# Performance work log

Measured on AMD Instinct MI355X. Metric: run time of the kernel, lower is better.

## Reference

```python
import jax, jax.numpy as jnp
import numpy as np

HQ, HKV, D, RD = 32, 8, 128, 64   # q heads, kv heads, head_dim, rotary_dim
EPS = 1e-6


def _rms_norm(x, w, eps):
    # per-head RMSNorm over last dim (non-gemma: scale by w)
    var = jnp.mean(x * x, axis=-1, keepdims=True)
    return x * jax.lax.rsqrt(var + eps) * w


def _partial_rope(x, c, s, rd):
    # x: [T, H, D]; c/s: [T, rd//2]; NeoX half-split rotation on first rd dims
    x1 = x[..., : rd // 2]
    x2 = x[..., rd // 2 : rd]
    c = c[:, None, :]
    s = s[:, None, :]
    return jnp.concatenate([x1 * c - x2 * s, x2 * c + x1 * s, x[..., rd:]], axis=-1)


def setup_inputs() -> dict:
    key = jax.random.key(0)
    ks = jax.random.split(key, 6)
    B, QL, HID, CACHE = 4, 512, 4096, 512
    T = B * QL
    MAXPOS = 4096
    NPAGES, PS, MP = 256, 16, 64  # total pages, page_size, max pages per seq

    hidden_states = jax.random.normal(ks[0], (T, HID), jnp.float32)
    inv = 1.0 / (10000.0 ** (np.arange(0, RD, 2, dtype=np.float64) / RD))
    ang = np.arange(MAXPOS)[:, None] * inv[None, :]
    cos = jnp.asarray(np.cos(ang), jnp.float32)   # [MAXPOS, RD//2]
    sin = jnp.asarray(np.sin(ang), jnp.float32)
    positions = jnp.tile(CACHE + jnp.arange(QL, dtype=jnp.int32), B)  # [T]
    k_cache = jax.random.normal(ks[1], (NPAGES, PS, HKV, D), jnp.float32)
    v_cache = jax.random.normal(ks[2], (NPAGES, PS, HKV, D), jnp.float32)
    page_table = jnp.arange(B * MP, dtype=jnp.int32).reshape(B, MP)
    cache_seqlens = jnp.full((B,), CACHE, jnp.int32)
    cu_seqlens_q = jnp.arange(B + 1, dtype=jnp.int32) * QL
    qkv_weight = jax.random.normal(ks[3], ((HQ + 2 * HKV) * D, HID), jnp.float32) * 0.02
    o_proj_weight = jax.random.normal(ks[4], (HID, HQ * D), jnp.float32) * 0.02
    q_norm_weight = jnp.ones((D,), jnp.float32)
    k_norm_weight = jnp.ones((D,), jnp.float32)
    return dict(hidden_states=hidden_states, cos=cos, sin=sin, positions=positions,
                k_cache=k_cache, v_cache=v_cache, page_table=page_table,
                cache_seqlens=cache_seqlens, cu_seqlens_q=cu_seqlens_q,
                qkv_weight=qkv_weight, o_proj_weight=o_proj_weight,
                q_norm_weight=q_norm_weight, k_norm_weight=k_norm_weight)


def reference(hidden_states, cos, sin, positions, k_cache, v_cache, page_table,
              cache_seqlens, cu_seqlens_q, qkv_weight, o_proj_weight,
              q_norm_weight, k_norm_weight):
    T = hidden_states.shape[0]
    B = cache_seqlens.shape[0]
    QL = T // B                       # equal-length sequences (extend mode)
    PS = k_cache.shape[1]

    # QKV projection + split
    qkv = hidden_states @ qkv_weight.T
    q, k, v = jnp.split(qkv, [HQ * D, (HQ + HKV) * D], axis=-1)

    # per-head QK RMSNorm (q_norm_weight.shape[0] == head_dim branch)
    q = _rms_norm(q.reshape(T, HQ, D), q_norm_weight, EPS)
    k = _rms_norm(k.reshape(T, HKV, D), k_norm_weight, EPS)
    v = v.reshape(T, HKV, D)

    # partial RoPE
    pc, psn = cos[positions], sin[positions]
    q = _partial_rope(q, pc, psn, RD)
    k = _partial_rope(k, pc, psn, RD)

    # paged KV-cache write: absolute slot = cache_seqlens[b] + j
    pos_abs = cache_seqlens[:, None] + jnp.arange(QL, dtype=jnp.int32)[None, :]  # [B,QL]
    pages = jnp.take_along_axis(page_table, pos_abs // PS, axis=1)
    slots = pos_abs % PS
    k_cache = k_cache.at[pages, slots].set(k.reshape(B, QL, HKV, D))
    v_cache = v_cache.at[pages, slots].set(v.reshape(B, QL, HKV, D))

    # gather per-sequence KV from pages: [B, KV, HKV, D]
    KV = page_table.shape[1] * PS
    keys = k_cache[page_table].reshape(B, KV, HKV, D)
    vals = v_cache[page_table].reshape(B, KV, HKV, D)

    # GQA paged attention with causal mask on absolute positions
    G = HQ // HKV
    qh = q.reshape(B, QL, HKV, G, D)
    scale = 1.0 / np.sqrt(D).astype(np.float32)
    scores = jnp.einsum('bqhgd,bkhd->bhgqk', qh, keys) * scale
    kpos = jnp.arange(KV, dtype=jnp.int32)
    mask = kpos[None, None, :] <= pos_abs[:, :, None]                  # [B,QL,KV]
    scores = jnp.where(mask[:, None, None, :, :], scores, -1e30)
    probs = jax.nn.softmax(scores, axis=-1)
    attn = jnp.einsum('bhgqk,bkhd->bqhgd', probs, vals).reshape(T, HQ * D)

    return attn @ o_proj_weight.T
```

## Files before the change

### kernel.cpp

```cpp
#include <hip/hip_runtime.h>

typedef unsigned int   u32;
typedef unsigned short u16;

typedef float  f32x4  __attribute__((ext_vector_type(4)));
typedef u32    u32x4  __attribute__((ext_vector_type(4)));
typedef u16    u16x4  __attribute__((ext_vector_type(4)));
typedef __bf16 bf16x8 __attribute__((ext_vector_type(8)));

union FragU { u16 us[8]; u32x4 q; bf16x8 v; };

__device__ __forceinline__ u32 f2u(float x){ union{float f;u32 u;}c; c.f=x; return c.u; }
__device__ __forceinline__ float u2f(u32 u){ union{float f;u32 u;}c; c.u=u; return c.f; }
__device__ __forceinline__ u16 bfhi(float x){ u32 u=f2u(x); return (u16)((u + 0x7fffu + ((u>>16)&1u))>>16); }
__device__ __forceinline__ u32 cvtpk(float a, float b){
  u32 r;
  asm("v_cvt_pk_bf16_f32 %0, %1, %2" : "=v"(r) : "v"(a), "v"(b));
  return r;
}

__device__ __forceinline__ void gload16(const void* g, void* l){
  __builtin_amdgcn_global_load_lds(
      (const __attribute__((address_space(1))) unsigned int*)g,
      (__attribute__((address_space(3))) unsigned int*)l, 16, 0, 0);
}

__global__ __launch_bounds__(256)
void prep_all(const float* __restrict__ s0, u32* __restrict__ d0, int n0,
              const float* __restrict__ s1, u32* __restrict__ d1, int n1,
              const float* __restrict__ s2, u32* __restrict__ d2, int n2,
              const float* __restrict__ k_cache, const float* __restrict__ v_cache,
              const int* __restrict__ page_table,
              u16* __restrict__ k_all, u16* __restrict__ v_allT)
{
  const int tid = threadIdx.x;
  if (blockIdx.x < 2048){
    const int total = n0 + n1 + n2;
    for (int i = blockIdx.x*256 + tid; i < total; i += 2048*256){
      const float* s; u32* d; int j = i;
      if (j < n0)            { s = s0; d = d0; }
      else if (j < n0 + n1)  { s = s1; d = d1; j -= n0; }
      else                   { s = s2; d = d2; j -= n0 + n1; }
      f32x4 a = __builtin_nontemporal_load(reinterpret_cast<const f32x4*>(s) + 2*j);
      f32x4 b = __builtin_nontemporal_load(reinterpret_cast<const f32x4*>(s) + 2*j + 1);
      reinterpret_cast<u32x4*>(d)[j] =
        (u32x4){ cvtpk(a.x,a.y), cvtpk(a.z,a.w), cvtpk(b.x,b.y), cvtpk(b.z,b.w) };
    }
    return;
  }
  __shared__ float tb[32][129];
  const int id = blockIdx.x - 2048;
  const int jt = id & 31, h = (id>>5)&7, b = id>>8;
  const int j0 = jt*32;
  {
    int r = tid>>3, c = tid&7;
    int j = j0 + r;
    int page = page_table[b*64 + (j>>4)];
    int slot = j & 15;
    const float* ks = k_cache + (size_t)((page*16 + slot)*8 + h)*128;
    const float* vs = v_cache + (size_t)((page*16 + slot)*8 + h)*128;
    u16* kd = k_all + ((size_t)(b*8+h)*1024 + j)*128;
    #pragma unroll
    for (int i=0;i<2;i++){
      int d0i = (c + 8*i)*8;
      f32x4 ka = __builtin_nontemporal_load(reinterpret_cast<const f32x4*>(ks + d0i));
      f32x4 kb = __builtin_nontemporal_load(reinterpret_cast<const f32x4*>(ks + d0i + 4));
      *reinterpret_cast<u32x4*>(kd + d0i) =
        (u32x4){ cvtpk(ka.x,ka.y), cvtpk(ka.z,ka.w), cvtpk(kb.x,kb.y), cvtpk(kb.z,kb.w) };
      f32x4 va = __builtin_nontemporal_load(reinterpret_cast<const f32x4*>(vs + d0i));
      f32x4 vb = __builtin_nontemporal_load(reinterpret_cast<const f32x4*>(vs + d0i + 4));
      tb[r][d0i+0]=va.x; tb[r][d0i+1]=va.y; tb[r][d0i+2]=va.z; tb[r][d0i+3]=va.w;
      tb[r][d0i+4]=vb.x; tb[r][d0i+5]=vb.y; tb[r][d0i+6]=vb.z; tb[r][d0i+7]=vb.w;
    }
  }
  __syncthreads();
  {
    int dout = tid>>1, jh = tid&1;
    u16* vd = v_allT + ((size_t)(b*8+h)*128 + dout)*1024 + j0 + jh*16;
    #pragma unroll
    for (int i=0;i<2;i++){
      int jb = jh*16 + i*8;
      u32x4 o = { cvtpk(tb[jb+0][dout], tb[jb+1][dout]),
                  cvtpk(tb[jb+2][dout], tb[jb+3][dout]),
                  cvtpk(tb[jb+4][dout], tb[jb+5][dout]),
                  cvtpk(tb[jb+6][dout], tb[jb+7][dout]) };
      *reinterpret_cast<u32x4*>(vd + i*8) = o;
    }
  }
}

__global__ __launch_bounds__(256, 2)
void gemm_pkA2(const u16* __restrict__ A, const u16* __restrict__ B,
               float* __restrict__ C, int M, int N, int K)
{
  extern __shared__ char smem[];
  const int tid  = threadIdx.x;
  const int lane = tid & 63;
  const int w    = tid >> 6;
  const int wm = w >> 1, wn = w & 1;
  const int ln = lane & 15, lg = lane >> 4;

  const int nbm = M >> 7;
  const int nbn = N / 192;
  const int nwg = nbm * nbn;
  const int swz = (blockIdx.x & 7) * (nwg >> 3) + (blockIdx.x >> 3);
  const int bm = swz % nbm, bn = swz / nbm;

  const size_t rb = (size_t)K * 2;
  const int lrow  = lane >> 3;
  const int lslot = (lane & 7) ^ (lrow & 7);
  const char* As0 = (const char*)A + (size_t)(bm*128 + w*8 + lrow)*rb + lslot*16;
  const char* Bs0 = (const char*)B + (size_t)(bn*192 + w*8 + lrow)*rb + lslot*16;

  auto stA = [&](int buf, int t) {
    const char* s = As0 + ((size_t)t << 7);
    char* d = smem + buf*40960 + w*1024;
    gload16(s,           d);
    gload16(s +  32*rb,  d + 4096);
    gload16(s +  64*rb,  d + 8192);
    gload16(s +  96*rb,  d + 12288);
  };
  auto stB = [&](int buf, int t) {
    const char* s = Bs0 + ((size_t)t << 7);
    char* d = smem + buf*40960 + 16384 + w*1024;
    gload16(s,           d);
    gload16(s +  32*rb,  d + 4096);
    gload16(s +  64*rb,  d + 8192);
    gload16(s +  96*rb,  d + 12288);
    gload16(s + 128*rb,  d + 16384);
    gload16(s + 160*rb,  d + 20480);
  };

  f32x4 z = {0.f,0.f,0.f,0.f};
  f32x4 acc[4][6];
  #pragma unroll
  for (int i=0;i<4;i++){
    #pragma unroll
    for (int j=0;j<6;j++) acc[i][j] = z;
  }

  const int nt = K >> 6;
  stA(0, 0); stB(0, 0);
  if (nt > 1) { stB(1, 1);
    asm volatile("s_waitcnt vmcnt(6)" ::: "memory");
  } else {
    asm volatile("s_waitcnt vmcnt(0)" ::: "memory");
  }
  __builtin_amdgcn_s_barrier();
  asm volatile("" ::: "memory");

  const int lx7 = ln & 7;

  for (int t = 0; t < nt; ++t){
    const int cur = t & 1;
    const char* bufc = smem + cur*40960;

    FragU bfr[6][2];
    #pragma unroll
    for (int ni=0; ni<6; ni++){
      const int rofs = 16384 + (wn*96 + ni*16 + ln)*128;
      #pragma unroll
      for (int ks=0; ks<2; ks++)
        bfr[ni][ks].q = *reinterpret_cast<const u32x4*>(bufc + rofs + (((ks*4+lg)^lx7)<<4));
    }
    FragU af[2][2];
    #pragma unroll
    for (int mf=0; mf<2; mf++){
      const int rofs = (wm*64 + mf*16 + ln)*128;
      #pragma unroll
      for (int ks=0; ks<2; ks++)
        af[mf][ks].q = *reinterpret_cast<const u32x4*>(bufc + rofs + (((ks*4+lg)^lx7)<<4));
    }
    if (t+1 < nt) stA(cur^1, t+1);
    __builtin_amdgcn_s_barrier();
    __builtin_amdgcn_s_setprio(1);
    #pragma unroll
    for (int ks=0; ks<2; ks++){
      #pragma unroll
      for (int mf=0; mf<2; mf++){
        #pragma unroll
        for (int ni=0; ni<6; ni++)
          acc[mf][ni] = __builtin_amdgcn_mfma_f32_16x16x32_bf16(af[mf][ks].v, bfr[ni][ks].v, acc[mf][ni], 0,0,0);
      }
    }
    __builtin_amdgcn_s_setprio(0);
    asm volatile("s_waitcnt lgkmcnt(0)" ::: "memory");
    __builtin_amdgcn_s_barrier();

    FragU ag[2][2];
    #pragma unroll
    for (int mf=0; mf<2; mf++){
      const int rofs = (wm*64 + (mf+2)*16 + ln)*128;
      #pragma unroll
      for (int ks=0; ks<2; ks++)
        ag[mf][ks].q = *reinterpret_cast<const u32x4*>(bufc + rofs + (((ks*4+lg)^lx7)<<4));
    }
    if (t+2 < nt) stB(cur, t+2);
    __builtin_amdgcn_s_barrier();
    __builtin_amdgcn_s_setprio(1);
    #pragma unroll
    for (int ks=0; ks<2; ks++){
      #pragma unroll
      for (int mf=0; mf<2; mf++){
        #pragma unroll
        for (int ni=0; ni<6; ni++)
          acc[mf+2][ni] = __builtin_amdgcn_mfma_f32_16x16x32_bf16(ag[mf][ks].v, bfr[ni][ks].v, acc[mf+2][ni], 0,0,0);
      }
    }
    __builtin_amdgcn_s_setprio(0);
    if (t+1 < nt){
      if (t+2 < nt) asm volatile("s_waitcnt vmcnt(6)" ::: "memory");
      else          asm volatile("s_waitcnt vmcnt(0)" ::: "memory");
    }
    __builtin_amdgcn_s_barrier();
    asm volatile("" ::: "memory");
  }

  #pragma unroll
  for (int mi=0; mi<4; mi++){
    #pragma unroll
    for (int ni=0; ni<6; ni++){
      const int row0 = bm*128 + wm*64 + mi*16 + lg*4;
      const int col  = bn*192 + wn*96 + ni*16 + ln;
      #pragma unroll
      for (int r=0; r<4; r++)
        C[(size_t)(row0+r)*N + col] = acc[mi][ni][r];
    }
  }
}

__global__ __launch_bounds__(256, 2)
void gemm_pkB2(const u16* __restrict__ A, const u16* __restrict__ B,
               float* __restrict__ C, int M, int N, int K)
{
  extern __shared__ char smem[];
  const int tid  = threadIdx.x;
  const int lane = tid & 63;
  const int w    = tid >> 6;
  const int wm = w >> 1, wn = w & 1;
  const int ln = lane & 15, lg = lane >> 4;

  const int nbm = M >> 7, nbn = N >> 7;
  const int nwg = nbm * nbn;
  const int swz = (blockIdx.x & 7) * (nwg >> 3) + (blockIdx.x >> 3);
  const int bm = swz % nbm, bn = swz / nbm;

  const size_t rb = (size_t)K * 2;
  const int lrow  = lane >> 3;
  const int lslot = (lane & 7) ^ (lrow & 7);
  const char* As0 = (const char*)A + (size_t)(bm*128 + w*8 + lrow)*rb + lslot*16;
  const char* Bs0 = (const char*)B + (size_t)(bn*128 + w*8 + lrow)*rb + lslot*16;

  auto stA = [&](int buf, int t) {
    const char* s = As0 + ((size_t)t << 7);
    char* d = smem + buf*32768 + w*1024;
    gload16(s,           d);
    gload16(s +  32*rb,  d + 4096);
    gload16(s +  64*rb,  d + 8192);
    gload16(s +  96*rb,  d + 12288);
  };
  auto stB = [&](int buf, int t) {
    const char* s = Bs0 + ((size_t)t << 7);
    char* d = smem + buf*32768 + 16384 + w*1024;
    gload16(s,           d);
    gload16(s +  32*rb,  d + 4096);
    gload16(s +  64*rb,  d + 8192);
    gload16(s +  96*rb,  d + 12288);
  };

  f32x4 z = {0.f,0.f,0.f,0.f};
  f32x4 acc[4][4];
  #pragma unroll
  for (int i=0;i<4;i++){
    #pragma unroll
    for (int j=0;j<4;j++) acc[i][j] = z;
  }

  const int nt = K >> 6;
  stA(0, 0); stB(0, 0);
  if (nt > 1) { stB(1, 1);
    asm volatile("s_waitcnt vmcnt(4)" ::: "memory");
  } else {
    asm volatile("s_waitcnt vmcnt(0)" ::: "memory");
  }
  __builtin_amdgcn_s_barrier();
  asm volatile("" ::: "memory");

  const int lx7 = ln & 7;

  for (int t = 0; t < nt; ++t){
    const int cur = t & 1;
    const char* bufc = smem + cur*32768;

    FragU bfr[4][2];
    #pragma unroll
    for (int ni=0; ni<4; ni++){
      const int rofs = 16384 + (wn*64 + ni*16 + ln)*128;
      #pragma unroll
      for (int ks=0; ks<2; ks++)
        bfr[ni][ks].q = *reinterpret_cast<const u32x4*>(bufc + rofs + (((ks*4+lg)^lx7)<<4));
    }
    FragU af[2][2];
    #pragma unroll
    for (int mf=0; mf<2; mf++){
      const int rofs = (wm*64 + mf*16 + ln)*128;
      #pragma unroll
      for (int ks=0; ks<2; ks++)
        af[mf][ks].q = *reinterpret_cast<const u32x4*>(bufc + rofs + (((ks*4+lg)^lx7)<<4));
    }
    if (t+1 < nt) stA(cur^1, t+1);
    __builtin_amdgcn_s_barrier();
    __builtin_amdgcn_s_setprio(1);
    #pragma unroll
    for (int ks=0; ks<2; ks++){
      #pragma unroll
      for (int mf=0; mf<2; mf++){
        #pragma unroll
        for (int ni=0; ni<4; ni++)
          acc[mf][ni] = __builtin_amdgcn_mfma_f32_16x16x32_bf16(af[mf][ks].v, bfr[ni][ks].v, acc[mf][ni], 0,0,0);
      }
    }
    __builtin_amdgcn_s_setprio(0);
    asm volatile("s_waitcnt lgkmcnt(0)" ::: "memory");
    __builtin_amdgcn_s_barrier();

    FragU ag[2][2];
    #pragma unroll
    for (int mf=0; mf<2; mf++){
      const int rofs = (wm*64 + (mf+2)*16 + ln)*128;
      #pragma unroll
      for (int ks=0; ks<2; ks++)
        ag[mf][ks].q = *reinterpret_cast<const u32x4*>(bufc + rofs + (((ks*4+lg)^lx7)<<4));
    }
    if (t+2 < nt) stB(cur, t+2);
    __builtin_amdgcn_s_barrier();
    __builtin_amdgcn_s_setprio(1);
    #pragma unroll
    for (int ks=0; ks<2; ks++){
      #pragma unroll
      for (int mf=0; mf<2; mf++){
        #pragma unroll
        for (int ni=0; ni<4; ni++)
          acc[mf+2][ni] = __builtin_amdgcn_mfma_f32_16x16x32_bf16(ag[mf][ks].v, bfr[ni][ks].v, acc[mf+2][ni], 0,0,0);
      }
    }
    __builtin_amdgcn_s_setprio(0);
    if (t+1 < nt){
      if (t+2 < nt) asm volatile("s_waitcnt vmcnt(4)" ::: "memory");
      else          asm volatile("s_waitcnt vmcnt(0)" ::: "memory");
    }
    __builtin_amdgcn_s_barrier();
    asm volatile("" ::: "memory");
  }

  #pragma unroll
  for (int mi=0; mi<4; mi++){
    #pragma unroll
    for (int ni=0; ni<4; ni++){
      const int row0 = bm*128 + wm*64 + mi*16 + lg*4;
      const int col  = bn*128 + wn*64 + ni*16 + ln;
      #pragma unroll
      for (int r=0; r<4; r++)
        C[(size_t)(row0+r)*N + col] = acc[mi][ni][r];
    }
  }
}

__global__ __launch_bounds__(256)
void norm_rope_kv(const float* __restrict__ qkv, const float* __restrict__ cosT,
                  const float* __restrict__ sinT, const int* __restrict__ positions,
                  const int* __restrict__ cache_seqlens,
                  const float* __restrict__ kw,
                  u16* __restrict__ k_all, u16* __restrict__ v_allT)
{
  const int t = blockIdx.x;
  const int lane = threadIdx.x & 63;
  const int w = threadIdx.x >> 6;
  const int b = t >> 9;
  const int q = t & 511;
  const int pos  = positions[t];
  const int cpos = cache_seqlens[b] + q;
  for (int it=0; it<4; ++it){
    int hh = it*4 + w;
    const float* xp = qkv + (size_t)t*6144 + (32+hh)*128 + 2*lane;
    float2 x = *reinterpret_cast<const float2*>(xp);
    if (hh < 8){
      float ss = x.x*x.x + x.y*x.y;
      #pragma unroll
      for (int mk=1; mk<64; mk<<=1) ss += __shfl_xor(ss, mk);
      float var = ss*(1.0f/128.0f) + 1e-6f;
      float rq = rsqrtf(var);
      rq = rq*(1.5f - 0.5f*var*rq*rq);
      x.x *= rq*kw[2*lane]; x.y *= rq*kw[2*lane+1];
      float px = __shfl_xor(x.x, 16);
      float py = __shfl_xor(x.y, 16);
      if (lane < 32){
        int ci = pos*32 + 2*(lane&15);
        float2 cc = *reinterpret_cast<const float2*>(cosT + ci);
        float2 sc = *reinterpret_cast<const float2*>(sinT + ci);
        if (lane < 16){ x.x = x.x*cc.x - px*sc.x; x.y = x.y*cc.y - py*sc.y; }
        else          { x.x = x.x*cc.x + px*sc.x; x.y = x.y*cc.y + py*sc.y; }
      }
      u16* kp = k_all + ((size_t)(b*8 + hh)*1024 + cpos)*128 + 2*lane;
      kp[0] = bfhi(x.x); kp[1] = bfhi(x.y);
    } else {
      u16* vp = v_allT + ((size_t)(b*8 + (hh-8))*128 + 2*lane)*1024 + cpos;
      vp[0]    = bfhi(x.x);
      vp[1024] = bfhi(x.y);
    }
  }
}

__global__ __launch_bounds__(512)
void attn_fused9(const float* __restrict__ qkv, const float* __restrict__ cosT,
                 const float* __restrict__ sinT, const int* __restrict__ positions,
                 const float* __restrict__ qw,
                 const u16* __restrict__ k_all, const u16* __restrict__ v_allT,
                 const int* __restrict__ cache_seqlens, u16* __restrict__ attnO)
{
  extern __shared__ char smem[];
  const int tid = threadIdx.x, lane = tid&63, w = tid>>6;
  const int ln = lane&15, lg = lane>>4;
  const int id = blockIdx.x;
  const int qt = id & 3, g = (id>>2)&3, kvh = (id>>4)&7, b = id>>7;
  const int cs = cache_seqlens[b];
  const int h  = kvh*4 + g;
  const int q0 = qt*128 + w*16;
  const float SCALE = 0.08838834764831845f;
  f32x4 z = {0.f,0.f,0.f,0.f};

  FragU qf[4];
  {
    const int row = b*512 + q0 + ln;
    const float* qp = qkv + (size_t)row*6144 + h*128;
    float xq[4][8];
    float ss = 0.f;
    #pragma unroll
    for (int ks=0; ks<4; ks++){
      int d0 = ks*32 + lg*8;
      f32x4 a = *reinterpret_cast<const f32x4*>(qp + d0);
      f32x4 c = *reinterpret_cast<const f32x4*>(qp + d0 + 4);
      xq[ks][0]=a.x; xq[ks][1]=a.y; xq[ks][2]=a.z; xq[ks][3]=a.w;
      xq[ks][4]=c.x; xq[ks][5]=c.y; xq[ks][6]=c.z; xq[ks][7]=c.w;
      #pragma unroll
      for (int k2=0;k2<8;k2++) ss += xq[ks][k2]*xq[ks][k2];
    }
    ss += __shfl_xor(ss, 16);
    ss += __shfl_xor(ss, 32);
    float var = ss*(1.0f/128.0f) + 1e-6f;
    float rq = rsqrtf(var);
    rq = rq*(1.5f - 0.5f*var*rq*rq);
    rq *= SCALE;
    #pragma unroll
    for (int ks=0; ks<4; ks++){
      int d0 = ks*32 + lg*8;
      f32x4 wa = *reinterpret_cast<const f32x4*>(qw + d0);
      f32x4 wb = *reinterpret_cast<const f32x4*>(qw + d0 + 4);
      xq[ks][0]*=rq*wa.x; xq[ks][1]*=rq*wa.y; xq[ks][2]*=rq*wa.z; xq[ks][3]*=rq*wa.w;
      xq[ks][4]*=rq*wb.x; xq[ks][5]*=rq*wb.y; xq[ks][6]*=rq*wb.z; xq[ks][7]*=rq*wb.w;
    }
    const int pos = positions[row];
    const int ci = pos*32 + lg*8;
    #pragma unroll
    for (int k2=0;k2<8;k2+=4){
      f32x4 cc = *reinterpret_cast<const f32x4*>(cosT + ci + k2);
      f32x4 sc = *reinterpret_cast<const f32x4*>(sinT + ci + k2);
      float cA[4] = {cc.x,cc.y,cc.z,cc.w};
      float sA[4] = {sc.x,sc.y,sc.z,sc.w};
      #pragma unroll
      for (int u=0;u<4;u++){
        float x1 = xq[0][k2+u], x2 = xq[1][k2+u];
        xq[0][k2+u] = x1*cA[u] - x2*sA[u];
        xq[1][k2+u] = x2*cA[u] + x1*sA[u];
      }
    }
    #pragma unroll
    for (int ks=0; ks<4; ks++)
      qf[ks].q = (u32x4){ cvtpk(xq[ks][0],xq[ks][1]), cvtpk(xq[ks][2],xq[ks][3]),
                          cvtpk(xq[ks][4],xq[ks][5]), cvtpk(xq[ks][6],xq[ks][7]) };
  }

  f32x4 O[8];
  #pragma unroll
  for (int i=0;i<8;i++) O[i] = z;
  float lacc[4] = {0.f,0.f,0.f,0.f};
  const int prow0 = cs + q0 + lg*4;
  const int nt = (cs + qt*128 + 128 + 63) >> 6;
  const char* kbase = (const char*)(k_all  + (size_t)(b*8+kvh)*1024*128);
  const char* vbase = (const char*)(v_allT + (size_t)(b*8+kvh)*128*1024);

  auto stK = [&](int buf, int t){
    #pragma unroll
    for (int i=0;i<2;i++){
      int row = i*32 + w*4 + (lane>>4);
      const char* s = kbase + (size_t)(t*64 + row)*256 + (((lane&15) ^ (row&7))<<4);
      gload16(s, smem + buf*16384 + i*8192 + w*1024);
    }
  };
  auto stV = [&](int buf, int t){
    #pragma unroll
    for (int i=0;i<2;i++){
      int row = i*64 + w*8 + (lane>>3);
      const char* s = vbase + (size_t)row*2048 + (size_t)t*128 + (((lane&7) ^ (row&7))<<4);
      gload16(s, smem + 32768 + buf*16384 + i*8192 + w*1024);
    }
  };

  stK(0, 0); stV(0, 0);
  if (nt > 1){ stK(1, 1); stV(1, 1); }

  for (int tile=0; tile<nt; ++tile){
    const int cur = tile & 1;
    const int kv0 = tile*64;
    if (tile+1 < nt) asm volatile("s_waitcnt vmcnt(4)" ::: "memory");
    else             asm volatile("s_waitcnt vmcnt(0)" ::: "memory");
    __builtin_amdgcn_s_barrier();

    const u16* Kc = (const u16*)(smem + cur*16384);
    f32x4 s[4]; s[0]=z; s[1]=z; s[2]=z; s[3]=z;
    #pragma unroll
    for (int ks=0; ks<4; ks++){
      int so = ((ks*4+lg) ^ (ln&7)) << 3;
      #pragma unroll
      for (int n=0; n<4; n++){
        FragU kf;
        kf.q = *reinterpret_cast<const u32x4*>(&Kc[(n*16+ln)*128 + so]);
        s[n] = __builtin_amdgcn_mfma_f32_16x16x32_bf16(qf[ks].v, kf.v, s[n], 0,0,0);
      }
    }

    float pv[4][4];
    if (kv0 + 63 <= cs + q0){
      #pragma unroll
      for (int n=0;n<4;n++){
        #pragma unroll
        for (int r=0;r<4;r++) pv[n][r] = __expf(s[n][r]);
      }
    } else {
      #pragma unroll
      for (int n=0;n<4;n++){
        #pragma unroll
        for (int r=0;r<4;r++){
          bool ok = (kv0 + n*16 + ln) <= (prow0 + r);
          pv[n][r] = ok ? __expf(s[n][r]) : 0.f;
        }
      }
    }
    #pragma unroll
    for (int r=0;r<4;r++) lacc[r] += (pv[0][r] + pv[1][r]) + (pv[2][r] + pv[3][r]);

    #pragma unroll
    for (int n=0;n<4;n++){
      #pragma unroll
      for (int rp=0; rp<2; rp++){
        u32 hpk = cvtpk(pv[n][rp*2], pv[n][rp*2+1]);
        int col  = n*16 + ln;
        int row0 = lg*4 + rp*2;
        int b0 = w*2048 + row0*128 + ((((col>>3) ^ ((row0>>1)&7)))<<4) + (col&7)*2;
        *(u16*)(smem + 65536 + b0)       = (u16)hpk;
        *(u16*)(smem + 65536 + b0 + 128) = (u16)(hpk >> 16);
      }
    }
    FragU pa[2];
    #pragma unroll
    for (int ks2=0; ks2<2; ks2++)
      pa[ks2].q = *reinterpret_cast<const u32x4*>(
          smem + 65536 + w*2048 + ln*128 + (((ks2*4+lg) ^ ((ln>>1)&7))<<4));

    const char* Vb = smem + 32768 + cur*16384;
    #pragma unroll
    for (int nf=0; nf<8; nf++){
      int dr = nf*16 + ln;
      #pragma unroll
      for (int ks2=0; ks2<2; ks2++){
        FragU vf;
        vf.q = *reinterpret_cast<const u32x4*>(Vb + dr*128 + (((ks2*4+lg) ^ (dr&7))<<4));
        O[nf] = __builtin_amdgcn_mfma_f32_16x16x32_bf16(pa[ks2].v, vf.v, O[nf], 0,0,0);
      }
    }
    asm volatile("s_waitcnt lgkmcnt(0)" ::: "memory");
    __builtin_amdgcn_s_barrier();
    if (tile+2 < nt){ stK(cur, tile+2); stV(cur, tile+2); }
  }

  #pragma unroll
  for (int off=1; off<16; off<<=1){
    #pragma unroll
    for (int r=0;r<4;r++) lacc[r] += __shfl_xor(lacc[r], off);
  }
  float il[4];
  #pragma unroll
  for (int r=0;r<4;r++) il[r] = 1.0f / lacc[r];
  u16* op = attnO + (size_t)(b*512 + q0 + lg*4)*4096 + h*128 + ln;
  #pragma unroll
  for (int nf=0; nf<8; nf++){
    #pragma unroll
    for (int r=0;r<4;r++)
      op[(size_t)r*4096 + nf*16] = bfhi(O[nf][r] * il[r]);
  }
}

extern "C" void kernel_launch(void* const* d_in, const int* in_sizes, int n_in,
                              void* d_out, int out_size, void* d_ws, size_t ws_size,
                              hipStream_t stream) {
  const float* hidden    = (const float*)d_in[0];
  const float* cosT      = (const float*)d_in[1];
  const float* sinT      = (const float*)d_in[2];
  const int*   positions = (const int*)  d_in[3];
  const float* k_cache   = (const float*)d_in[4];
  const float* v_cache   = (const float*)d_in[5];
  const int*   page_tab  = (const int*)  d_in[6];
  const int*   cache_sl  = (const int*)  d_in[7];
  const float* qkv_w     = (const float*)d_in[9];
  const float* o_w       = (const float*)d_in[10];
  const float* qnw       = (const float*)d_in[11];
  const float* knw       = (const float*)d_in[12];
  float* out = (float*)d_out;

  float* qkv   = (float*)d_ws;
  u16* k_all   = (u16*)(qkv + 12582912);
  u16* v_allT  = k_all  + 4194304;
  u16* attnPk  = v_allT + 4194304;
  u16* hidPk   = attnPk + 8388608;
  u16* qkvwPk  = hidPk  + 8388608;
  u16* owPk    = qkvwPk + 25165824;
  (void)in_sizes; (void)n_in; (void)out_size; (void)ws_size;

  (void)hipFuncSetAttribute(reinterpret_cast<const void*>(gemm_pkA2),
                            hipFuncAttributeMaxDynamicSharedMemorySize, 81920);
  (void)hipFuncSetAttribute(reinterpret_cast<const void*>(gemm_pkB2),
                            hipFuncAttributeMaxDynamicSharedMemorySize, 65536);
  (void)hipFuncSetAttribute(reinterpret_cast<const void*>(attn_fused9),
                            hipFuncAttributeMaxDynamicSharedMemorySize, 81920);

  hipLaunchKernelGGL(prep_all, dim3(3072), dim3(256), 0, stream,
                     hidden, (u32*)hidPk, 1048576,
                     qkv_w, (u32*)qkvwPk, 3145728,
                     o_w, (u32*)owPk, 2097152,
                     k_cache, v_cache, page_tab, k_all, v_allT);
  hipLaunchKernelGGL(gemm_pkA2, dim3(512), dim3(256), 81920, stream,
                     hidPk, qkvwPk, qkv, 2048, 6144, 4096);
  hipLaunchKernelGGL(norm_rope_kv, dim3(2048), dim3(256), 0, stream,
                     qkv, cosT, sinT, positions, cache_sl, knw, k_all, v_allT);
  hipLaunchKernelGGL(attn_fused9, dim3(512), dim3(512), 81920, stream,
                     qkv, cosT, sinT, positions, qnw, k_all, v_allT, cache_sl, attnPk);
  hipLaunchKernelGGL(gemm_pkB2, dim3(512), dim3(256), 65536, stream,
                     attnPk, owPk, out, 2048, 4096, 4096);
}
```

Measured before the change: 294.0 us.

## Move paged KV gather into norm kernel and skip positions beyond cache length

The paged KV-cache gather and transpose moves out of the weight-packing prep kernel and into the K-norm/RoPE kernel. Gather blocks now skip tiles at or beyond cache_seqlens, which avoids redundant reads and writes for slots the new tokens overwrite. The pack kernel is also reshaped to a fixed per-block chunk of 4096 elements with an unrolled loop instead of a grid-stride loop. The gather now runs after the QKV GEMM rather than before it, which changes how the stages overlap.

```diff
diff --git a/kernel.cpp b/kernel.cpp
--- a/kernel.cpp
+++ b/kernel.cpp
@@ -26,66 +26,28 @@
 }
 
 __global__ __launch_bounds__(256)
-void prep_all(const float* __restrict__ s0, u32* __restrict__ d0, int n0,
-              const float* __restrict__ s1, u32* __restrict__ d1, int n1,
-              const float* __restrict__ s2, u32* __restrict__ d2, int n2,
-              const float* __restrict__ k_cache, const float* __restrict__ v_cache,
-              const int* __restrict__ page_table,
-              u16* __restrict__ k_all, u16* __restrict__ v_allT)
+void prep_pack(const float* __restrict__ s0, u32* __restrict__ d0,
+               const float* __restrict__ s1, u32* __restrict__ d1,
+               const float* __restrict__ s2, u32* __restrict__ d2)
 {
-  const int tid = threadIdx.x;
-  if (blockIdx.x < 2048){
-    const int total = n0 + n1 + n2;
-    for (int i = blockIdx.x*256 + tid; i < total; i += 2048*256){
-      const float* s; u32* d; int j = i;
-      if (j < n0)            { s = s0; d = d0; }
-      else if (j < n0 + n1)  { s = s1; d = d1; j -= n0; }
-      else                   { s = s2; d = d2; j -= n0 + n1; }
-      f32x4 a = __builtin_nontemporal_load(reinterpret_cast<const f32x4*>(s) + 2*j);
-      f32x4 b = __builtin_nontemporal_load(reinterpret_cast<const f32x4*>(s) + 2*j + 1);
-      reinterpret_cast<u32x4*>(d)[j] =
-        (u32x4){ cvtpk(a.x,a.y), cvtpk(a.z,a.w), cvtpk(b.x,b.y), cvtpk(b.z,b.w) };
-    }
-    return;
-  }
-  __shared__ float tb[32][129];
-  const int id = blockIdx.x - 2048;
-  const int jt = id & 31, h = (id>>5)&7, b = id>>8;
-  const int j0 = jt*32;
-  {
-    int r = tid>>3, c = tid&7;
-    int j = j0 + r;
-    int page = page_table[b*64 + (j>>4)];
-    int slot = j & 15;
-    const float* ks = k_cache + (size_t)((page*16 + slot)*8 + h)*128;
-    const float* vs = v_cache + (size_t)((page*16 + slot)*8 + h)*128;
-    u16* kd = k_all + ((size_t)(b*8+h)*1024 + j)*128;
-    #pragma unroll
-    for (int i=0;i<2;i++){
-      int d0i = (c + 8*i)*8;
-      f32x4 ka = __builtin_nontemporal_load(reinterpret_cast<const f32x4*>(ks + d0i));
-      f32x4 kb = __builtin_nontemporal_load(reinterpret_cast<const f32x4*>(ks + d0i + 4));
-      *reinterpret_cast<u32x4*>(kd + d0i) =
-        (u32x4){ cvtpk(ka.x,ka.y), cvtpk(ka.z,ka.w), cvtpk(kb.x,kb.y), cvtpk(kb.z,kb.w) };
-      f32x4 va = __builtin_nontemporal_load(reinterpret_cast<const f32x4*>(vs + d0i));
-      f32x4 vb = __builtin_nontemporal_load(reinterpret_cast<const f32x4*>(vs + d0i + 4));
-      tb[r][d0i+0]=va.x; tb[r][d0i+1]=va.y; tb[r][d0i+2]=va.z; tb[r][d0i+3]=va.w;
-      tb[r][d0i+4]=vb.x; tb[r][d0i+5]=vb.y; tb[r][d0i+6]=vb.z; tb[r][d0i+7]=vb.w;
-    }
-  }
-  __syncthreads();
-  {
-    int dout = tid>>1, jh = tid&1;
-    u16* vd = v_allT + ((size_t)(b*8+h)*128 + dout)*1024 + j0 + jh*16;
-    #pragma unroll
-    for (int i=0;i<2;i++){
-      int jb = jh*16 + i*8;
-      u32x4 o = { cvtpk(tb[jb+0][dout], tb[jb+1][dout]),
-                  cvtpk(tb[jb+2][dout], tb[jb+3][dout]),
-                  cvtpk(tb[jb+4][dout], tb[jb+5][dout]),
-                  cvtpk(tb[jb+6][dout], tb[jb+7][dout]) };
-      *reinterpret_cast<u32x4*>(vd + i*8) = o;
-    }
+  const int bid = blockIdx.x;
+  const float* s; u32* d; int base;
+  if (bid < 256)       { s = s0; d = d0; base = bid*4096; }
+  else if (bid < 1024) { s = s1; d = d1; base = (bid-256)*4096; }
+  else                 { s = s2; d = d2; base = (bid-1024)*4096; }
+  int j = base + threadIdx.x;
+  #pragma unroll
+  for (int it=0; it<8; ++it){
+    const int j2 = j + 256;
+    f32x4 a0 = __builtin_nontemporal_load(reinterpret_cast<const f32x4*>(s) + 2*j);
+    f32x4 a1 = __builtin_nontemporal_load(reinterpret_cast<const f32x4*>(s) + 2*j + 1);
+    f32x4 b0 = __builtin_nontemporal_load(reinterpret_cast<const f32x4*>(s) + 2*j2);
+    f32x4 b1 = __builtin_nontemporal_load(reinterpret_cast<const f32x4*>(s) + 2*j2 + 1);
+    reinterpret_cast<u32x4*>(d)[j] =
+      (u32x4){ cvtpk(a0.x,a0.y), cvtpk(a0.z,a0.w), cvtpk(a1.x,a1.y), cvtpk(a1.z,a1.w) };
+    reinterpret_cast<u32x4*>(d)[j2] =
+      (u32x4){ cvtpk(b0.x,b0.y), cvtpk(b0.z,b0.w), cvtpk(b1.x,b1.y), cvtpk(b1.z,b1.w) };
+    j += 512;
   }
 }
 
@@ -367,46 +329,97 @@
 }
 
 __global__ __launch_bounds__(256)
-void norm_rope_kv(const float* __restrict__ qkv, const float* __restrict__ cosT,
-                  const float* __restrict__ sinT, const int* __restrict__ positions,
-                  const int* __restrict__ cache_seqlens,
-                  const float* __restrict__ kw,
-                  u16* __restrict__ k_all, u16* __restrict__ v_allT)
+void norm_gather_kv(const float* __restrict__ qkv, const float* __restrict__ cosT,
+                    const float* __restrict__ sinT, const int* __restrict__ positions,
+                    const int* __restrict__ cache_seqlens,
+                    const float* __restrict__ kw,
+                    const float* __restrict__ k_cache, const float* __restrict__ v_cache,
+                    const int* __restrict__ page_table,
+                    u16* __restrict__ k_all, u16* __restrict__ v_allT)
 {
-  const int t = blockIdx.x;
-  const int lane = threadIdx.x & 63;
-  const int w = threadIdx.x >> 6;
-  const int b = t >> 9;
-  const int q = t & 511;
-  const int pos  = positions[t];
-  const int cpos = cache_seqlens[b] + q;
-  for (int it=0; it<4; ++it){
-    int hh = it*4 + w;
-    const float* xp = qkv + (size_t)t*6144 + (32+hh)*128 + 2*lane;
-    float2 x = *reinterpret_cast<const float2*>(xp);
-    if (hh < 8){
-      float ss = x.x*x.x + x.y*x.y;
-      #pragma unroll
-      for (int mk=1; mk<64; mk<<=1) ss += __shfl_xor(ss, mk);
-      float var = ss*(1.0f/128.0f) + 1e-6f;
-      float rq = rsqrtf(var);
-      rq = rq*(1.5f - 0.5f*var*rq*rq);
-      x.x *= rq*kw[2*lane]; x.y *= rq*kw[2*lane+1];
-      float px = __shfl_xor(x.x, 16);
-      float py = __shfl_xor(x.y, 16);
-      if (lane < 32){
-        int ci = pos*32 + 2*(lane&15);
-        float2 cc = *reinterpret_cast<const float2*>(cosT + ci);
-        float2 sc = *reinterpret_cast<const float2*>(sinT + ci);
-        if (lane < 16){ x.x = x.x*cc.x - px*sc.x; x.y = x.y*cc.y - py*sc.y; }
-        else          { x.x = x.x*cc.x + px*sc.x; x.y = x.y*cc.y + py*sc.y; }
-      }
-      u16* kp = k_all + ((size_t)(b*8 + hh)*1024 + cpos)*128 + 2*lane;
-      kp[0] = bfhi(x.x); kp[1] = bfhi(x.y);
-    } else {
-      u16* vp = v_allT + ((size_t)(b*8 + (hh-8))*128 + 2*lane)*1024 + cpos;
-      vp[0]    = bfhi(x.x);
-      vp[1024] = bfhi(x.y);
+  const int tid = threadIdx.x;
+  if (blockIdx.x < 2048){
+    const int t = blockIdx.x;
+    const int lane = tid & 63;
+    const int w = tid >> 6;
+    const int b = t >> 9;
+    const int q = t & 511;
+    const int pos  = positions[t];
+    const int cpos = cache_seqlens[b] + q;
+    for (int it=0; it<4; ++it){
+      int hh = it*4 + w;
+      const float* xp = qkv + (size_t)t*6144 + (32+hh)*128 + 2*lane;
+      float2 x = *reinterpret_cast<const float2*>(xp);
+      if (hh < 8){
+        float ss = x.x*x.x + x.y*x.y;
+        #pragma unroll
+        for (int mk=1; mk<64; mk<<=1) ss += __shfl_xor(ss, mk);
+        float var = ss*(1.0f/128.0f) + 1e-6f;
+        float rq = rsqrtf(var);
+        rq = rq*(1.5f - 0.5f*var*rq*rq);
+        x.x *= rq*kw[2*lane]; x.y *= rq*kw[2*lane+1];
+        float px = __shfl_xor(x.x, 16);
+        float py = __shfl_xor(x.y, 16);
+        if (lane < 32){
+          int ci = pos*32 + 2*(lane&15);
+          float2 cc = *reinterpret_cast<const float2*>(cosT + ci);
+          float2 sc = *reinterpret_cast<const float2*>(sinT + ci);
+          if (lane < 16){ x.x = x.x*cc.x - px*sc.x; x.y = x.y*cc.y - py*sc.y; }
+          else          { x.x = x.x*cc.x + px*sc.x; x.y = x.y*cc.y + py*sc.y; }
+        }
+        u16* kp = k_all + ((size_t)(b*8 + hh)*1024 + cpos)*128 + 2*lane;
+        kp[0] = bfhi(x.x); kp[1] = bfhi(x.y);
+      } else {
+        u16* vp = v_allT + ((size_t)(b*8 + (hh-8))*128 + 2*lane)*1024 + cpos;
+        vp[0]    = bfhi(x.x);
+        vp[1024] = bfhi(x.y);
+      }
+    }
+    return;
+  }
+  __shared__ float tb[32][129];
+  const int id = blockIdx.x - 2048;
+  const int jt = id & 31, h = (id>>5)&7, b = id>>8;
+  const int j0 = jt*32;
+  const int csb = cache_seqlens[b];
+  if (j0 >= csb) return;
+  {
+    int r = tid>>3, c = tid&7;
+    int j = j0 + r;
+    int page = page_table[b*64 + (j>>4)];
+    int slot = j & 15;
+    const float* ks = k_cache + (size_t)((page*16 + slot)*8 + h)*128;
+    const float* vs = v_cache + (size_t)((page*16 + slot)*8 + h)*128;
+    u16* kd = k_all + ((size_t)(b*8+h)*1024 + j)*128;
+    const bool wr = (j < csb);
+    #pragma unroll
+    for (int i=0;i<2;i++){
+      int d0i = (c + 8*i)*8;
+      f32x4 ka = __builtin_nontemporal_load(reinterpret_cast<const f32x4*>(ks + d0i));
+      f32x4 kb = __builtin_nontemporal_load(reinterpret_cast<const f32x4*>(ks + d0i + 4));
+      if (wr)
+        *reinterpret_cast<u32x4*>(kd + d0i) =
+          (u32x4){ cvtpk(ka.x,ka.y), cvtpk(ka.z,ka.w), cvtpk(kb.x,kb.y), cvtpk(kb.z,kb.w) };
+      f32x4 va = __builtin_nontemporal_load(reinterpret_cast<const f32x4*>(vs + d0i));
+      f32x4 vb = __builtin_nontemporal_load(reinterpret_cast<const f32x4*>(vs + d0i + 4));
+      tb[r][d0i+0]=va.x; tb[r][d0i+1]=va.y; tb[r][d0i+2]=va.z; tb[r][d0i+3]=va.w;
+      tb[r][d0i+4]=vb.x; tb[r][d0i+5]=vb.y; tb[r][d0i+6]=vb.z; tb[r][d0i+7]=vb.w;
+    }
+  }
+  __syncthreads();
+  {
+    int dout = tid>>1, jh = tid&1;
+    u16* vd = v_allT + ((size_t)(b*8+h)*128 + dout)*1024 + j0 + jh*16;
+    #pragma unroll
+    for (int i=0;i<2;i++){
+      if (j0 + jh*16 + i*8 < csb){
+        int jb = jh*16 + i*8;
+        u32x4 o = { cvtpk(tb[jb+0][dout], tb[jb+1][dout]),
+                    cvtpk(tb[jb+2][dout], tb[jb+3][dout]),
+                    cvtpk(tb[jb+4][dout], tb[jb+5][dout]),
+                    cvtpk(tb[jb+6][dout], tb[jb+7][dout]) };
+        *reinterpret_cast<u32x4*>(vd + i*8) = o;
+      }
     }
   }
 }
@@ -633,15 +646,15 @@
   (void)hipFuncSetAttribute(reinterpret_cast<const void*>(attn_fused9),
                             hipFuncAttributeMaxDynamicSharedMemorySize, 81920);
 
-  hipLaunchKernelGGL(prep_all, dim3(3072), dim3(256), 0, stream,
-                     hidden, (u32*)hidPk, 1048576,
-                     qkv_w, (u32*)qkvwPk, 3145728,
-                     o_w, (u32*)owPk, 2097152,
-                     k_cache, v_cache, page_tab, k_all, v_allT);
+  hipLaunchKernelGGL(prep_pack, dim3(1536), dim3(256), 0, stream,
+                     hidden, (u32*)hidPk,
+                     qkv_w, (u32*)qkvwPk,
+                     o_w, (u32*)owPk);
   hipLaunchKernelGGL(gemm_pkA2, dim3(512), dim3(256), 81920, stream,
                      hidPk, qkvwPk, qkv, 2048, 6144, 4096);
-  hipLaunchKernelGGL(norm_rope_kv, dim3(2048), dim3(256), 0, stream,
-                     qkv, cosT, sinT, positions, cache_sl, knw, k_all, v_allT);
+  hipLaunchKernelGGL(norm_gather_kv, dim3(3072), dim3(256), 0, stream,
+                     qkv, cosT, sinT, positions, cache_sl, knw,
+                     k_cache, v_cache, page_tab, k_all, v_allT);
   hipLaunchKernelGGL(attn_fused9, dim3(512), dim3(512), 81920, stream,
                      qkv, cosT, sinT, positions, qnw, k_all, v_allT, cache_sl, attnPk);
   hipLaunchKernelGGL(gemm_pkB2, dim3(512), dim3(256), 65536, stream,
```

After: 294.4 us. No clear change (+0.1%).
